# Performance work log

Measured on AMD Instinct MI355X. Metric: run time of the kernel, lower is better.

Reference implementation:

```python
import jax, jax.numpy as jnp
import numpy as np

NEG_INF = -1e30  # stand-in for float('-inf') masked_fill (safe for softmax)


def setup_inputs() -> dict:
    key = jax.random.key(0)
    ks = jax.random.split(key, 7)
    B, T, C, H, D = 4, 2048, 64, 6, 64
    s = 1.0 / np.sqrt(C)
    return {
        "x": jax.random.normal(ks[0], (B, T, C), dtype=jnp.float32),
        "y": jax.random.normal(ks[1], (B, T, C), dtype=jnp.float32),
        "Wq": jax.random.normal(ks[2], (H, C, D), dtype=jnp.float32) * s,
        "Wk": jax.random.normal(ks[3], (H, C, D), dtype=jnp.float32) * s,
        "Wv": jax.random.normal(ks[4], (H, C, D), dtype=jnp.float32) * s,
        "W_proj": jax.random.normal(ks[5], (H * D, C), dtype=jnp.float32) * (1.0 / np.sqrt(H * D)),
        "b_proj": jnp.zeros((C,), dtype=jnp.float32),
    }


def reference(x, y, Wq, Wk, Wv, W_proj, b_proj):
    # x, y: [B, T, C]; per-head projections stacked over H (heads vectorized).
    B, T, C = x.shape
    H, _, D = Wq.shape
    q = jnp.einsum("btc,hcd->bhtd", x, Wq)   # query from decoder input x
    k = jnp.einsum("btc,hcd->bhtd", y, Wk)   # key from encoder output y
    v = jnp.einsum("btc,hcd->bhtd", y, Wv)
    scale = D ** (-0.5)
    wei = jnp.einsum("bhtd,bhsd->bhts", q, k) * scale  # [B,H,T,T]
    # triu(ones(T,T), diagonal=1) future mask (causal)
    future = jnp.triu(jnp.ones((T, T), dtype=bool), k=1)
    wei = jnp.where(future, NEG_INF, wei)
    wei = jax.nn.softmax(wei, axis=-1)  # dropout = identity in eval
    out = jnp.einsum("bhts,bhsd->bhtd", wei, v)          # [B,H,T,D]
    out = out.transpose(0, 2, 1, 3).reshape(B, T, H * D)  # concat heads
    return out @ W_proj + b_proj                          # [B,T,C]
```

## Files before the change

kernel.cpp:

```cpp
#include <hip/hip_runtime.h>


typedef unsigned short u16t;
typedef __attribute__((ext_vector_type(8))) short short8;
typedef __attribute__((ext_vector_type(4))) float float4v;

#define MFMA16(a, b, c) __builtin_amdgcn_mfma_f32_16x16x32_bf16((a), (b), (c), 0, 0, 0)

union U8 { short8 s; unsigned u[4]; };

__device__ __forceinline__ float fexp2(float x) {
  return __builtin_amdgcn_exp2f(x);
}
__device__ __forceinline__ float bf2f(u16t u) {
  return __uint_as_float(((unsigned)u) << 16);
}
__device__ __forceinline__ u16t f2bf(float f) {
  unsigned u = __float_as_uint(f);
  u += 0x7fffu + ((u >> 16) & 1u);
  return (u16t)(u >> 16);
}
__device__ __forceinline__ unsigned bftr(float f) {
  return __float_as_uint(f) >> 16;
}
__device__ __forceinline__ short8 load8_f32_bf16(const float* p) {
  float4 f0 = *(const float4*)p;
  float4 f1 = *(const float4*)(p + 4);
  short8 r;
  r[0] = (short)f2bf(f0.x); r[1] = (short)f2bf(f0.y);
  r[2] = (short)f2bf(f0.z); r[3] = (short)f2bf(f0.w);
  r[4] = (short)f2bf(f1.x); r[5] = (short)f2bf(f1.y);
  r[6] = (short)f2bf(f1.z); r[7] = (short)f2bf(f1.w);
  return r;
}

constexpr int Bb = 4, Tt = 2048, Cc = 64, Hh = 6, Dd = 64;
constexpr int BH = Bb * Hh;
constexpr int NQT = Tt / 64;
constexpr int LDT = 72;
constexpr int OST = 65;
#define QSCALE (0.125f * 1.44269504088896f)

__global__ __launch_bounds__(256) void qkv_kernel(
    const float* __restrict__ x, const float* __restrict__ y,
    const float* __restrict__ Wq, const float* __restrict__ Wk,
    const float* __restrict__ Wv,
    u16t* __restrict__ Q, u16t* __restrict__ K, u16t* __restrict__ Vt) {
  __shared__ __align__(16) u16t wtq[64 * LDT];
  __shared__ __align__(16) u16t wtk[64 * LDT];
  __shared__ __align__(16) u16t wtv[64 * LDT];

  int bid = blockIdx.x;
  int bh = bid >> 5, tt = bid & 31;
  int b = bh / Hh, h = bh - b * Hh;
  int tid = threadIdx.x;
  int w = tid >> 6, lane = tid & 63;
  int l15 = lane & 15, q4 = lane >> 4;

  {
    const float4* wq4 = (const float4*)(Wq + h * 4096);
    const float4* wk4 = (const float4*)(Wk + h * 4096);
    const float4* wv4 = (const float4*)(Wv + h * 4096);
#pragma unroll
    for (int i = 0; i < 4; ++i) {
      int fidx = tid + i * 256;
      float4 qv = wq4[fidx], kv = wk4[fidx], vv = wv4[fidx];
      int base = fidx * 4;
      int c = base >> 6, d0 = base & 63;
      wtq[(d0 + 0) * LDT + c] = f2bf(qv.x);
      wtq[(d0 + 1) * LDT + c] = f2bf(qv.y);
      wtq[(d0 + 2) * LDT + c] = f2bf(qv.z);
      wtq[(d0 + 3) * LDT + c] = f2bf(qv.w);
      wtk[(d0 + 0) * LDT + c] = f2bf(kv.x);
      wtk[(d0 + 1) * LDT + c] = f2bf(kv.y);
      wtk[(d0 + 2) * LDT + c] = f2bf(kv.z);
      wtk[(d0 + 3) * LDT + c] = f2bf(kv.w);
      wtv[(d0 + 0) * LDT + c] = f2bf(vv.x);
      wtv[(d0 + 1) * LDT + c] = f2bf(vv.y);
      wtv[(d0 + 2) * LDT + c] = f2bf(vv.z);
      wtv[(d0 + 3) * LDT + c] = f2bf(vv.w);
    }
  }

  int trow = tt * 64 + w * 16 + l15;
  const float* xrow = x + ((size_t)b * Tt + trow) * Cc;
  const float* yrow = y + ((size_t)b * Tt + trow) * Cc;
  short8 xa[2], ya[2];
#pragma unroll
  for (int kc = 0; kc < 2; ++kc) {
    xa[kc] = load8_f32_bf16(xrow + kc * 32 + q4 * 8);
    ya[kc] = load8_f32_bf16(yrow + kc * 32 + q4 * 8);
  }
  __syncthreads();

  float4v qa4[4], ka4[4], va4[4];
#pragma unroll
  for (int nc = 0; nc < 4; ++nc) {
    qa4[nc] = (float4v){0.f, 0.f, 0.f, 0.f};
    ka4[nc] = (float4v){0.f, 0.f, 0.f, 0.f};
    va4[nc] = (float4v){0.f, 0.f, 0.f, 0.f};
  }
#pragma unroll
  for (int nc = 0; nc < 4; ++nc) {
#pragma unroll
    for (int kc = 0; kc < 2; ++kc) {
      int off = (nc * 16 + l15) * LDT + kc * 32 + q4 * 8;
      short8 bq = *(const short8*)&wtq[off];
      short8 bk = *(const short8*)&wtk[off];
      short8 bv = *(const short8*)&wtv[off];
      qa4[nc] = MFMA16(xa[kc], bq, qa4[nc]);
      ka4[nc] = MFMA16(ya[kc], bk, ka4[nc]);
      va4[nc] = MFMA16(ya[kc], bv, va4[nc]);
    }
  }
  __syncthreads();

#pragma unroll
  for (int reg = 0; reg < 4; ++reg) {
    int rloc = w * 16 + q4 * 4 + reg;
#pragma unroll
    for (int nc = 0; nc < 4; ++nc) {
      wtq[rloc * LDT + nc * 16 + l15] = f2bf(qa4[nc][reg] * QSCALE);
      wtk[rloc * LDT + nc * 16 + l15] = f2bf(ka4[nc][reg]);
      wtv[(nc * 16 + l15) * LDT + rloc] = f2bf(va4[nc][reg]);
    }
  }
  __syncthreads();

  size_t tilebase = ((size_t)bh * Tt + tt * 64) * Dd;
#pragma unroll
  for (int i = 0; i < 2; ++i) {
    int id = tid * 2 + i;
    int row = id >> 3, c8 = id & 7;
    *(uint4*)&Q[tilebase + row * 64 + c8 * 8] = *(const uint4*)&wtq[row * LDT + c8 * 8];
    *(uint4*)&K[tilebase + row * 64 + c8 * 8] = *(const uint4*)&wtk[row * LDT + c8 * 8];
    *(uint4*)&Vt[((size_t)bh * 64 + row) * Tt + tt * 64 + c8 * 8] =
        *(const uint4*)&wtv[row * LDT + c8 * 8];
  }
}

__global__ __launch_bounds__(256, 3) void attn_kernel(
    const u16t* __restrict__ Q, const u16t* __restrict__ K,
    const u16t* __restrict__ Vt, u16t* __restrict__ att) {
  __shared__ __align__(16) unsigned char smem[64 * LDT * 2 * 2 + 256];
  u16t* Kl = (u16t*)smem;
  u16t* Vl = (u16t*)(smem + 64 * LDT * 2);
  float* Ol = (float*)smem;
  float* Ll = (float*)(smem + 64 * LDT * 2 * 2);

  int bid = blockIdx.x;
  int bh = bid % BH;
  int qt = (NQT - 1) - bid / BH;
  int b = bh / Hh, h = bh - (bh / Hh) * Hh;
  int tid = threadIdx.x;
  int w = tid >> 6;
  int lane = tid & 63;
  int l15 = lane & 15, q4 = lane >> 4;

  short8 qf[4][2];
#pragma unroll
  for (int it = 0; it < 4; ++it) {
    const u16t* qb = Q + ((size_t)bh * Tt + qt * 64 + it * 16 + l15) * Dd;
    qf[it][0] = *(const short8*)(qb + q4 * 8);
    qf[it][1] = *(const short8*)(qb + 32 + q4 * 8);
  }

  float4v O[4][4];
#pragma unroll
  for (int it = 0; it < 4; ++it)
#pragma unroll
    for (int nc = 0; nc < 4; ++nc) O[it][nc] = (float4v){0.f, 0.f, 0.f, 0.f};
  float l_[4] = {0.f, 0.f, 0.f, 0.f};

  const u16t* Kbh = K + (size_t)bh * Tt * Dd;
  const u16t* Vbh = Vt + (size_t)bh * Dd * Tt;

  for (int jt = 0; jt <= qt; ++jt) {
    __syncthreads();
    {
      const u16t* ksrc = Kbh + (size_t)jt * 64 * 64;
      const u16t* vsrc = Vbh + jt * 64;
#pragma unroll
      for (int i = 0; i < 2; ++i) {
        int id = tid * 2 + i;
        int r = id >> 3, c8 = id & 7;
        *(uint4*)&Kl[r * LDT + c8 * 8] = *(const uint4*)(ksrc + r * 64 + c8 * 8);
        *(uint4*)&Vl[r * LDT + c8 * 8] = *(const uint4*)(vsrc + (size_t)r * Tt + c8 * 8);
      }
    }
    __syncthreads();

    short8 kf0 = *(const short8*)&Kl[(w * 16 + l15) * LDT + q4 * 8];
    short8 kf1 = *(const short8*)&Kl[(w * 16 + l15) * LDT + 32 + q4 * 8];
    short8 vf[4];
#pragma unroll
    for (int nc = 0; nc < 4; ++nc) {
      uint2 vv = *(const uint2*)&Vl[(nc * 16 + l15) * LDT + w * 16 + q4 * 4];
      U8 t;
      t.u[0] = vv.x; t.u[1] = vv.y; t.u[2] = 0u; t.u[3] = 0u;
      vf[nc] = t.s;
    }

    bool diag = (jt == qt);
#pragma unroll
    for (int it = 0; it < 4; ++it) {
      if (diag && w > it) continue;
      float4v S = (float4v){0.f, 0.f, 0.f, 0.f};
      S = MFMA16(kf0, qf[it][0], S);
      S = MFMA16(kf1, qf[it][1], S);
      float p[4];
#pragma unroll
      for (int reg = 0; reg < 4; ++reg) {
        p[reg] = (diag && w == it && (q4 * 4 + reg) > l15) ? 0.f : fexp2(S[reg]);
        l_[it] += p[reg];
      }
      U8 pa;
      pa.u[0] = bftr(p[0]) | (bftr(p[1]) << 16);
      pa.u[1] = bftr(p[2]) | (bftr(p[3]) << 16);
      pa.u[2] = 0u; pa.u[3] = 0u;
#pragma unroll
      for (int nc = 0; nc < 4; ++nc)
        O[it][nc] = MFMA16(pa.s, vf[nc], O[it][nc]);
    }
  }

#pragma unroll
  for (int it = 0; it < 4; ++it) {
    l_[it] += __shfl_xor(l_[it], 16);
    l_[it] += __shfl_xor(l_[it], 32);
  }

  __syncthreads();
#pragma unroll
  for (int r = 0; r < 4; ++r) {
#pragma unroll
    for (int itc = 0; itc < 4; ++itc) {
      if (((itc - w) & 3) == r) {
#pragma unroll
        for (int nc = 0; nc < 4; ++nc)
#pragma unroll
          for (int reg = 0; reg < 4; ++reg) {
            int addr = (itc * 16 + q4 * 4 + reg) * OST + nc * 16 + l15;
            if (r == 0) Ol[addr] = O[itc][nc][reg];
            else        Ol[addr] += O[itc][nc][reg];
          }
        if (q4 == 0) {
          if (r == 0) Ll[itc * 16 + l15] = l_[itc];
          else        Ll[itc * 16 + l15] += l_[itc];
        }
      }
    }
    __syncthreads();
  }

#pragma unroll
  for (int i = 0; i < 2; ++i) {
    int id = tid * 2 + i;
    int row = id >> 3, c8 = id & 7;
    float inv = 1.0f / Ll[row];
    const float* orow = &Ol[row * OST + c8 * 8];
    U8 o;
#pragma unroll
    for (int k = 0; k < 4; ++k)
      o.u[k] = f2bf(orow[2 * k] * inv) | ((unsigned)f2bf(orow[2 * k + 1] * inv) << 16);
    int t = qt * 64 + row;
    *(uint4*)&att[((size_t)b * Tt + t) * (Hh * Dd) + h * Dd + c8 * 8] = *(const uint4*)&o;
  }
}

constexpr int LDP = 392;

__global__ __launch_bounds__(256) void proj_kernel(
    const u16t* __restrict__ att, const float* __restrict__ Wp,
    const float* __restrict__ bp, float* __restrict__ out) {
  __shared__ __align__(16) u16t wpt[64 * LDP];

  int bid = blockIdx.x;
  int tid = threadIdx.x;
  int w = tid >> 6, lane = tid & 63;
  int l15 = lane & 15, q4 = lane >> 4;

  const float4* wp4 = (const float4*)Wp;
#pragma unroll
  for (int i = 0; i < 24; ++i) {
    int fidx = tid + i * 256;
    float4 v = wp4[fidx];
    int base = fidx * 4;
    int r = base >> 6, c0 = base & 63;
    wpt[(c0 + 0) * LDP + r] = f2bf(v.x);
    wpt[(c0 + 1) * LDP + r] = f2bf(v.y);
    wpt[(c0 + 2) * LDP + r] = f2bf(v.z);
    wpt[(c0 + 3) * LDP + r] = f2bf(v.w);
  }
  __syncthreads();

  int row0 = bid * 64 + w * 16;
  const u16t* arow = att + (size_t)(row0 + l15) * 384;

  float4v acc[4];
#pragma unroll
  for (int nc = 0; nc < 4; ++nc) acc[nc] = (float4v){0.f, 0.f, 0.f, 0.f};

#pragma unroll
  for (int kc = 0; kc < 12; ++kc) {
    short8 a = *(const short8*)(arow + kc * 32 + q4 * 8);
#pragma unroll
    for (int nc = 0; nc < 4; ++nc) {
      short8 bfr = *(const short8*)&wpt[(nc * 16 + l15) * LDP + kc * 32 + q4 * 8];
      acc[nc] = MFMA16(a, bfr, acc[nc]);
    }
  }

  float bv[4];
#pragma unroll
  for (int nc = 0; nc < 4; ++nc) bv[nc] = bp[nc * 16 + l15];
#pragma unroll
  for (int reg = 0; reg < 4; ++reg) {
    int t = row0 + q4 * 4 + reg;
    size_t obase = (size_t)t * 64;
#pragma unroll
    for (int nc = 0; nc < 4; ++nc)
      out[obase + nc * 16 + l15] = acc[nc][reg] + bv[nc];
  }
}

extern "C" void kernel_launch(void* const* d_in, const int* in_sizes, int n_in,
                              void* d_out, int out_size, void* d_ws, size_t ws_size,
                              hipStream_t stream) {
  const float* x  = (const float*)d_in[0];
  const float* y  = (const float*)d_in[1];
  const float* Wq = (const float*)d_in[2];
  const float* Wk = (const float*)d_in[3];
  const float* Wv = (const float*)d_in[4];
  const float* Wp = (const float*)d_in[5];
  const float* bp = (const float*)d_in[6];
  float* out = (float*)d_out;

  const size_t NBH = (size_t)BH * Tt * Dd;
  u16t* Qs   = (u16t*)d_ws;
  u16t* Ks   = Qs + NBH;
  u16t* Vts  = Ks + NBH;
  u16t* attb = Vts + NBH;

  qkv_kernel<<<BH * NQT, 256, 0, stream>>>(x, y, Wq, Wk, Wv, Qs, Ks, Vts);
  attn_kernel<<<BH * NQT, 256, 0, stream>>>(Qs, Ks, Vts, attb);
  proj_kernel<<<(Bb * Tt) / 64, 256, 0, stream>>>(attb, Wp, bp, out);
}
```

Before: 125.5 us.

## Process two key tiles per step with register prefetch and full-K PV MFMA

The attention loop now handles 128 keys per iteration. The two 64-key subtiles fill both halves of the 32-wide bf16 MFMA K dimension in the PV product, where the previous version zero-padded half of it. The next K/V block is prefetched into registers while the current block is computed, overlapping global loads with MFMA work. This halves the number of barriers and the count of PV MFMAs. In exchange it uses more registers and LDS, and the occupancy hint of 3 waves is dropped.

Result: slower. 158.3 us (+26.2%).

```diff
diff --git a/kernel.cpp b/kernel.cpp
--- a/kernel.cpp
+++ b/kernel.cpp
@@ -38,6 +38,7 @@
 constexpr int BH = Bb * Hh;
 constexpr int NQT = Tt / 64;
 constexpr int LDT = 72;
+constexpr int LDV = 136;
 constexpr int OST = 65;
 #define QSCALE (0.125f * 1.44269504088896f)
 
@@ -139,14 +140,14 @@
   }
 }
 
-__global__ __launch_bounds__(256, 3) void attn_kernel(
+__global__ __launch_bounds__(256) void attn_kernel(
     const u16t* __restrict__ Q, const u16t* __restrict__ K,
     const u16t* __restrict__ Vt, u16t* __restrict__ att) {
-  __shared__ __align__(16) unsigned char smem[64 * LDT * 2 * 2 + 256];
+  __shared__ __align__(16) unsigned char smem[128 * LDT * 2 + 64 * LDV * 2];
   u16t* Kl = (u16t*)smem;
-  u16t* Vl = (u16t*)(smem + 64 * LDT * 2);
+  u16t* Vl = (u16t*)(smem + 128 * LDT * 2);
   float* Ol = (float*)smem;
-  float* Ll = (float*)(smem + 64 * LDT * 2 * 2);
+  float* Ll = (float*)(smem + 64 * OST * 4);
 
   int bid = blockIdx.x;
   int bh = bid % BH;
@@ -174,50 +175,88 @@
 
   const u16t* Kbh = K + (size_t)bh * Tt * Dd;
   const u16t* Vbh = Vt + (size_t)bh * Dd * Tt;
-
-  for (int jt = 0; jt <= qt; ++jt) {
+  const int bsmax = qt >> 1;
+
+  uint4 pk[4], pv[4];
+#pragma unroll
+  for (int i = 0; i < 4; ++i) {
+    int id = tid + i * 256;
+    pk[i] = *(const uint4*)(Kbh + (size_t)(id >> 3) * 64 + (id & 7) * 8);
+    pv[i] = *(const uint4*)(Vbh + (size_t)(id >> 4) * Tt + (id & 15) * 8);
+  }
+
+  for (int bs = 0; bs <= bsmax; ++bs) {
     __syncthreads();
-    {
-      const u16t* ksrc = Kbh + (size_t)jt * 64 * 64;
-      const u16t* vsrc = Vbh + jt * 64;
-#pragma unroll
-      for (int i = 0; i < 2; ++i) {
-        int id = tid * 2 + i;
-        int r = id >> 3, c8 = id & 7;
-        *(uint4*)&Kl[r * LDT + c8 * 8] = *(const uint4*)(ksrc + r * 64 + c8 * 8);
-        *(uint4*)&Vl[r * LDT + c8 * 8] = *(const uint4*)(vsrc + (size_t)r * Tt + c8 * 8);
+#pragma unroll
+    for (int i = 0; i < 4; ++i) {
+      int id = tid + i * 256;
+      *(uint4*)&Kl[(id >> 3) * LDT + (id & 7) * 8] = pk[i];
+      *(uint4*)&Vl[(id >> 4) * LDV + (id & 15) * 8] = pv[i];
+    }
+    __syncthreads();
+    if (bs < bsmax) {
+      const u16t* ks = Kbh + (size_t)(bs + 1) * 128 * 64;
+      const u16t* vs = Vbh + (bs + 1) * 128;
+#pragma unroll
+      for (int i = 0; i < 4; ++i) {
+        int id = tid + i * 256;
+        pk[i] = *(const uint4*)(ks + (size_t)(id >> 3) * 64 + (id & 7) * 8);
+        pv[i] = *(const uint4*)(vs + (size_t)(id >> 4) * Tt + (id & 15) * 8);
       }
     }
-    __syncthreads();
-
-    short8 kf0 = *(const short8*)&Kl[(w * 16 + l15) * LDT + q4 * 8];
-    short8 kf1 = *(const short8*)&Kl[(w * 16 + l15) * LDT + 32 + q4 * 8];
+
+    bool d0 = (2 * bs == qt);
+    bool s1 = (2 * bs + 1 > qt);
+    bool d1 = (2 * bs + 1 == qt);
+
+    short8 kf00 = *(const short8*)&Kl[(w * 16 + l15) * LDT + q4 * 8];
+    short8 kf01 = *(const short8*)&Kl[(w * 16 + l15) * LDT + 32 + q4 * 8];
+    short8 kf10 = kf00, kf11 = kf01;
+    if (!s1) {
+      kf10 = *(const short8*)&Kl[(64 + w * 16 + l15) * LDT + q4 * 8];
+      kf11 = *(const short8*)&Kl[(64 + w * 16 + l15) * LDT + 32 + q4 * 8];
+    }
     short8 vf[4];
 #pragma unroll
     for (int nc = 0; nc < 4; ++nc) {
-      uint2 vv = *(const uint2*)&Vl[(nc * 16 + l15) * LDT + w * 16 + q4 * 4];
       U8 t;
-      t.u[0] = vv.x; t.u[1] = vv.y; t.u[2] = 0u; t.u[3] = 0u;
+      *(uint2*)&t.u[0] = *(const uint2*)&Vl[(nc * 16 + l15) * LDV + w * 16 + q4 * 4];
+      *(uint2*)&t.u[2] = *(const uint2*)&Vl[(nc * 16 + l15) * LDV + 64 + w * 16 + q4 * 4];
       vf[nc] = t.s;
     }
 
-    bool diag = (jt == qt);
 #pragma unroll
     for (int it = 0; it < 4; ++it) {
-      if (diag && w > it) continue;
-      float4v S = (float4v){0.f, 0.f, 0.f, 0.f};
-      S = MFMA16(kf0, qf[it][0], S);
-      S = MFMA16(kf1, qf[it][1], S);
-      float p[4];
+      if (d0 && w > it) continue;
+      float4v S0 = (float4v){0.f, 0.f, 0.f, 0.f};
+      S0 = MFMA16(kf00, qf[it][0], S0);
+      S0 = MFMA16(kf01, qf[it][1], S0);
+      bool m0 = d0 && (w == it);
+      float p0[4], p1[4];
 #pragma unroll
       for (int reg = 0; reg < 4; ++reg) {
-        p[reg] = (diag && w == it && (q4 * 4 + reg) > l15) ? 0.f : fexp2(S[reg]);
-        l_[it] += p[reg];
+        p0[reg] = (m0 && (q4 * 4 + reg) > l15) ? 0.f : fexp2(S0[reg]);
+        l_[it] += p0[reg];
+      }
+      if (s1 || (d1 && w > it)) {
+#pragma unroll
+        for (int reg = 0; reg < 4; ++reg) p1[reg] = 0.f;
+      } else {
+        float4v S1 = (float4v){0.f, 0.f, 0.f, 0.f};
+        S1 = MFMA16(kf10, qf[it][0], S1);
+        S1 = MFMA16(kf11, qf[it][1], S1);
+        bool m1 = d1 && (w == it);
+#pragma unroll
+        for (int reg = 0; reg < 4; ++reg) {
+          p1[reg] = (m1 && (q4 * 4 + reg) > l15) ? 0.f : fexp2(S1[reg]);
+          l_[it] += p1[reg];
+        }
       }
       U8 pa;
-      pa.u[0] = bftr(p[0]) | (bftr(p[1]) << 16);
-      pa.u[1] = bftr(p[2]) | (bftr(p[3]) << 16);
-      pa.u[2] = 0u; pa.u[3] = 0u;
+      pa.u[0] = bftr(p0[0]) | (bftr(p0[1]) << 16);
+      pa.u[1] = bftr(p0[2]) | (bftr(p0[3]) << 16);
+      pa.u[2] = bftr(p1[0]) | (bftr(p1[1]) << 16);
+      pa.u[3] = bftr(p1[2]) | (bftr(p1[3]) << 16);
 #pragma unroll
       for (int nc = 0; nc < 4; ++nc)
         O[it][nc] = MFMA16(pa.s, vf[nc], O[it][nc]);
```
